# Optimization experiments

Measured on AMD Instinct MI355X. Metric: run time of the kernel, lower is better.

The kernel has to match this reference:

```python
import jax, jax.numpy as jnp
import numpy as np

EMB = 768
HEADS = 12
HEAD_DIM = EMB // HEADS
SCALE = HEAD_DIM ** -0.5


def setup_inputs() -> dict:
    key = jax.random.key(0)
    kq, kk, kv, kw = jax.random.split(key, 4)
    B, H, N, D = 2, HEADS, 2048, HEAD_DIM
    queries = jax.random.normal(kq, (B, H, N, D), dtype=jnp.float32)
    keys = jax.random.normal(kk, (B, H, N, D), dtype=jnp.float32)
    values = jax.random.normal(kv, (B, H, N, D), dtype=jnp.float32)
    proj_w = jax.random.normal(kw, (EMB, EMB), dtype=jnp.float32) * (EMB ** -0.5)
    proj_b = jnp.zeros((EMB,), dtype=jnp.float32)
    return {"queries": queries, "keys": keys, "values": values,
            "proj_w": proj_w, "proj_b": proj_b}


def reference(queries, keys, values, proj_w, proj_b):
    # energy: [b, h, n, n] -- full quadratic score matrix, as in the original
    energy = jnp.einsum('bhij,bhkj->bhik', queries, keys) * SCALE
    att = jax.nn.softmax(energy, axis=-1)  # att_drop_p=0.0 -> identity
    out = jnp.einsum('bhij,bhjk->bhik', att, values)  # [b, h, n, d]
    b, h, n, d = out.shape
    out = jnp.transpose(out, (0, 2, 1, 3)).reshape(b, n, h * d)  # 'b h n d -> b n (h d)'
    # nn.Linear: x @ W^T + b (projection dropout is inference identity)
    return out @ proj_w.T + proj_b
```

## Files before the change

kernel.cpp:

```cpp
#include <hip/hip_runtime.h>
#include <cstdint>

typedef short bf16x8 __attribute__((ext_vector_type(8)));
typedef float f32x4 __attribute__((ext_vector_type(4)));
typedef uint16_t u16x4 __attribute__((ext_vector_type(4)));

#define MFMA_16x16x32(a, b, c) __builtin_amdgcn_mfma_f32_16x16x32_bf16((a), (b), (c), 0, 0, 0)

static constexpr int BATCH = 2;
static constexpr int HEADS = 12;
static constexpr int BH    = BATCH * HEADS;
static constexpr int NCTX  = 2048;
static constexpr int DH    = 64;
static constexpr int EMB   = 768;

static constexpr float QSCALE = 0.125f * 1.44269504088896340736f;

__device__ __forceinline__ uint16_t f2bf(float x) {
    uint32_t u = __float_as_uint(x);
    u += 0x7FFFu + ((u >> 16) & 1u);
    return (uint16_t)(u >> 16);
}
__device__ __forceinline__ uint32_t cvt_pk_bf16(float lo, float hi) {
    uint32_t r;
    asm("v_cvt_pk_bf16_f32 %0, %1, %2" : "=v"(r) : "v"(lo), "v"(hi));
    return r;
}

__global__ __launch_bounds__(256) void k_prep(
        const float* __restrict__ v, uint16_t* __restrict__ vt,
        const float* __restrict__ kf32, uint16_t* __restrict__ kb, int n4k,
        const float* __restrict__ w32, uint16_t* __restrict__ wb, int n4w) {
    const int bid = blockIdx.x;
    const int t   = threadIdx.x;

    if (bid < BH * (NCTX / 64)) {
        __shared__ uint16_t tileT[64][72];
        const int bh = bid >> 5;
        const int n0 = (bid & 31) * 64;

        const int r  = t >> 2;
        const int cc = (t & 3) * 16;
        const float* vp = v + ((size_t)bh * NCTX + n0 + r) * DH + cc;
#pragma unroll
        for (int u = 0; u < 4; ++u) {
            float4 x = reinterpret_cast<const float4*>(vp)[u];
            tileT[cc + 4 * u + 0][r] = f2bf(x.x);
            tileT[cc + 4 * u + 1][r] = f2bf(x.y);
            tileT[cc + 4 * u + 2][r] = f2bf(x.z);
            tileT[cc + 4 * u + 3][r] = f2bf(x.w);
        }
        __syncthreads();

        const int l2 = t & 63;
        const int s0 = t >> 6;
        const int gg = l2 >> 4;
        const int c2 = l2 & 15;
        uint16_t* vb = vt + ((size_t)bh * 32 + (n0 >> 6)) * 8 * 512;
#pragma unroll
        for (int u = 0; u < 2; ++u) {
            const int slot = s0 + 4 * u;
            const int f = slot >> 1, h = slot & 1;
            bf16x8 x = *reinterpret_cast<const bf16x8*>(&tileT[f * 16 + c2][h * 32 + 8 * gg]);
            *reinterpret_cast<bf16x8*>(vb + (size_t)slot * 512 + l2 * 8) = x;
        }
    } else {
        const int i = (bid - BH * (NCTX / 64)) * 256 + t;
        const float* src; uint16_t* dst; int j;
        if (i < n4k) { src = kf32; dst = kb; j = i; }
        else {
            j = i - n4k;
            if (j >= n4w) return;
            src = w32; dst = wb;
        }
        float4 x = reinterpret_cast<const float4*>(src)[j];
        u16x4 hv = {f2bf(x.x), f2bf(x.y), f2bf(x.z), f2bf(x.w)};
        reinterpret_cast<u16x4*>(dst)[j] = hv;
    }
}

__global__ __launch_bounds__(256) void k_attn(
        const float* __restrict__ q, const uint16_t* __restrict__ kb,
        const uint16_t* __restrict__ vf, uint16_t* __restrict__ xb) {
    const int bh = blockIdx.y;
    const int b  = bh / HEADS;
    const int h  = bh % HEADS;
    const int tid = threadIdx.x;
    const int w = tid >> 6;
    const int l = tid & 63;
    const int g = l >> 4;
    const int c = l & 15;

    __shared__ uint16_t K_s[2][64][72];
    __shared__ uint16_t P_s[4][16][72];

    const int q0 = blockIdx.x * 64 + w * 16;

    bf16x8 qa[2];
    {
        const float* qp = q + ((size_t)bh * NCTX + q0 + c) * DH + 8 * g;
#pragma unroll
        for (int kf = 0; kf < 2; ++kf) {
            float4 x0 = *reinterpret_cast<const float4*>(qp + kf * 32);
            float4 x1 = *reinterpret_cast<const float4*>(qp + kf * 32 + 4);
            bf16x8 f;
            f[0] = (short)f2bf(x0.x * QSCALE); f[1] = (short)f2bf(x0.y * QSCALE);
            f[2] = (short)f2bf(x0.z * QSCALE); f[3] = (short)f2bf(x0.w * QSCALE);
            f[4] = (short)f2bf(x1.x * QSCALE); f[5] = (short)f2bf(x1.y * QSCALE);
            f[6] = (short)f2bf(x1.z * QSCALE); f[7] = (short)f2bf(x1.w * QSCALE);
            qa[kf] = f;
        }
    }

    f32x4 zero = {0.f, 0.f, 0.f, 0.f};
    f32x4 o[4] = {zero, zero, zero, zero};
    float m = -1e30f;
    float lsum = 0.f;

    const int srow = tid >> 3;
    const int sch  = tid & 7;

    const uint16_t* kb_b = kb + (size_t)bh * NCTX * DH + srow * DH + sch * 8;
    const uint16_t* vf_b = vf + (size_t)bh * 32 * 8 * 512 + (size_t)l * 8;

    {
        bf16x8 a0 = *reinterpret_cast<const bf16x8*>(kb_b);
        bf16x8 a1 = *reinterpret_cast<const bf16x8*>(kb_b + 32 * DH);
        *reinterpret_cast<bf16x8*>(&K_s[0][srow][sch * 8])      = a0;
        *reinterpret_cast<bf16x8*>(&K_s[0][srow + 32][sch * 8]) = a1;
    }
    __syncthreads();

    for (int t = 0; t < NCTX / 64; ++t) {
        const int cur = t & 1;
        const int nxt = cur ^ 1;

        bf16x8 nk0, nk1;
        const bool pf = (t + 1) < NCTX / 64;
        if (pf) {
            const size_t ko = (size_t)(t + 1) * 64 * DH;
            nk0 = *reinterpret_cast<const bf16x8*>(kb_b + ko);
            nk1 = *reinterpret_cast<const bf16x8*>(kb_b + ko + 32 * DH);
        }

        bf16x8 vr[8];
#pragma unroll
        for (int s = 0; s < 8; ++s)
            vr[s] = *reinterpret_cast<const bf16x8*>(vf_b + ((size_t)t * 8 + s) * 512);

        f32x4 s[4] = {zero, zero, zero, zero};
        __builtin_amdgcn_s_setprio(1);
#pragma unroll
        for (int nf = 0; nf < 4; ++nf) {
#pragma unroll
            for (int kf = 0; kf < 2; ++kf) {
                bf16x8 bhf = *reinterpret_cast<const bf16x8*>(&K_s[cur][nf * 16 + c][kf * 32 + 8 * g]);
                s[nf] = MFMA_16x16x32(bhf, qa[kf], s[nf]);
            }
        }
        __builtin_amdgcn_s_setprio(0);

        float pm0 = fmaxf(fmaxf(s[0][0], s[0][1]), fmaxf(s[0][2], s[0][3]));
        float pm1 = fmaxf(fmaxf(s[1][0], s[1][1]), fmaxf(s[1][2], s[1][3]));
        float pm2 = fmaxf(fmaxf(s[2][0], s[2][1]), fmaxf(s[2][2], s[2][3]));
        float pm3 = fmaxf(fmaxf(s[3][0], s[3][1]), fmaxf(s[3][2], s[3][3]));
        float pmax = fmaxf(fmaxf(pm0, pm1), fmaxf(pm2, pm3));

        if (!__all(pmax <= m + 11.0f)) {
            float smax = fmaxf(pmax, __shfl_xor(pmax, 16));
            smax = fmaxf(smax, __shfl_xor(smax, 32));
            float mnew = fmaxf(m, smax);
            float corr = __builtin_amdgcn_exp2f(m - mnew);
            m = mnew;
            lsum *= corr;
#pragma unroll
            for (int r = 0; r < 4; ++r) {
                float cr = __shfl(corr, 4 * g + r);
#pragma unroll
                for (int f = 0; f < 4; ++f) o[f][r] *= cr;
            }
        }

#pragma unroll
        for (int nf = 0; nf < 4; ++nf) {
            float p0 = __builtin_amdgcn_exp2f(s[nf][0] - m);
            float p1 = __builtin_amdgcn_exp2f(s[nf][1] - m);
            float p2 = __builtin_amdgcn_exp2f(s[nf][2] - m);
            float p3 = __builtin_amdgcn_exp2f(s[nf][3] - m);
            lsum += (p0 + p1) + (p2 + p3);
            uint2 pk;
            pk.x = cvt_pk_bf16(p0, p1);
            pk.y = cvt_pk_bf16(p2, p3);
            *reinterpret_cast<uint2*>(&P_s[w][c][16 * nf + 4 * g]) = pk;
        }

        bf16x8 pa0 = *reinterpret_cast<const bf16x8*>(&P_s[w][c][8 * g]);
        bf16x8 pa1 = *reinterpret_cast<const bf16x8*>(&P_s[w][c][32 + 8 * g]);
        __builtin_amdgcn_s_setprio(1);
#pragma unroll
        for (int f = 0; f < 4; ++f) {
            o[f] = MFMA_16x16x32(pa0, vr[2 * f],     o[f]);
            o[f] = MFMA_16x16x32(pa1, vr[2 * f + 1], o[f]);
        }
        __builtin_amdgcn_s_setprio(0);

        if (pf) {
            *reinterpret_cast<bf16x8*>(&K_s[nxt][srow][sch * 8])      = nk0;
            *reinterpret_cast<bf16x8*>(&K_s[nxt][srow + 32][sch * 8]) = nk1;
        }
        __syncthreads();
    }

    lsum += __shfl_xor(lsum, 16);
    lsum += __shfl_xor(lsum, 32);
    const float linv = 1.0f / lsum;

    const size_t xbase = ((size_t)b * NCTX + q0) * EMB + h * DH;
#pragma unroll
    for (int r = 0; r < 4; ++r) {
        float lr = __shfl(linv, 4 * g + r);
#pragma unroll
        for (int f = 0; f < 4; ++f) {
            float v = o[f][r] * lr;
            size_t addr = xbase + (size_t)(4 * g + r) * EMB + f * 16 + c;
            xb[addr] = f2bf(v);
        }
    }
}

__global__ __launch_bounds__(256) void k_proj(
        const uint16_t* __restrict__ xb, const uint16_t* __restrict__ wb,
        const float* __restrict__ bias, float* __restrict__ out) {
    const int tid = threadIdx.x;
    const int w = tid >> 6;
    const int l = tid & 63;
    const int g = l >> 4;
    const int c = l & 15;
    const int m0 = blockIdx.x * 64 + w * 16;
    const int n0 = blockIdx.y * 64;

    __shared__ uint16_t W_s[64][72];

    f32x4 zero = {0.f, 0.f, 0.f, 0.f};
    f32x4 acc[4] = {zero, zero, zero, zero};

    const int srow = tid >> 2;
    const int sch  = tid & 3;
    constexpr int ROUNDS = EMB / 64;

    const uint16_t* whp = wb + (size_t)(n0 + srow) * EMB + sch * 8;
    const uint16_t* xhp = xb + (size_t)(m0 + c) * EMB + 8 * g;

    bf16x8 w0 = *reinterpret_cast<const bf16x8*>(whp);
    bf16x8 w1 = *reinterpret_cast<const bf16x8*>(whp + 32);
    bf16x8 a0 = *reinterpret_cast<const bf16x8*>(xhp);
    bf16x8 a1 = *reinterpret_cast<const bf16x8*>(xhp + 32);

    for (int rd = 0; rd < ROUNDS; ++rd) {
        __syncthreads();
        *reinterpret_cast<bf16x8*>(&W_s[srow][sch * 8])      = w0;
        *reinterpret_cast<bf16x8*>(&W_s[srow][32 + sch * 8]) = w1;
        __syncthreads();

        const int rn = (rd + 1 < ROUNDS) ? (rd + 1) : (ROUNDS - 1);
        bf16x8 w0n = *reinterpret_cast<const bf16x8*>(whp + (size_t)rn * 64);
        bf16x8 w1n = *reinterpret_cast<const bf16x8*>(whp + (size_t)rn * 64 + 32);
        bf16x8 a0n = *reinterpret_cast<const bf16x8*>(xhp + (size_t)rn * 64);
        bf16x8 a1n = *reinterpret_cast<const bf16x8*>(xhp + (size_t)rn * 64 + 32);

        __builtin_amdgcn_s_setprio(1);
#pragma unroll
        for (int nf = 0; nf < 4; ++nf) {
            bf16x8 b0 = *reinterpret_cast<const bf16x8*>(&W_s[nf * 16 + c][8 * g]);
            bf16x8 b1 = *reinterpret_cast<const bf16x8*>(&W_s[nf * 16 + c][32 + 8 * g]);
            acc[nf] = MFMA_16x16x32(a0, b0, acc[nf]);
            acc[nf] = MFMA_16x16x32(a1, b1, acc[nf]);
        }
        __builtin_amdgcn_s_setprio(0);

        w0 = w0n; w1 = w1n; a0 = a0n; a1 = a1n;
    }

#pragma unroll
    for (int nf = 0; nf < 4; ++nf) {
#pragma unroll
        for (int r = 0; r < 4; ++r) {
            int row = m0 + g * 4 + r;
            int col = n0 + nf * 16 + c;
            out[(size_t)row * EMB + col] = acc[nf][r] + bias[col];
        }
    }
}

extern "C" void kernel_launch(void* const* d_in, const int* in_sizes, int n_in,
                              void* d_out, int out_size, void* d_ws, size_t ws_size,
                              hipStream_t stream) {
    const float* q    = (const float*)d_in[0];
    const float* k    = (const float*)d_in[1];
    const float* v    = (const float*)d_in[2];
    const float* pw   = (const float*)d_in[3];
    const float* pb   = (const float*)d_in[4];
    float* out = (float*)d_out;

    const size_t nqkv = (size_t)BH * NCTX * DH;
    const size_t nx   = (size_t)BATCH * NCTX * EMB;
    const size_t nw   = (size_t)EMB * EMB;

    uint8_t* ws = (uint8_t*)d_ws;
    uint16_t* kb = (uint16_t*)ws;              ws += nqkv * 2;
    uint16_t* vf = (uint16_t*)ws;              ws += nqkv * 2;
    uint16_t* xb = (uint16_t*)ws;              ws += nx * 2;
    uint16_t* wb = (uint16_t*)ws;              ws += nw * 2;

    const int n4k = (int)(nqkv / 4);
    const int n4w = (int)(nw / 4);
    const int nprep = BH * (NCTX / 64) + (n4k + n4w + 255) / 256;
    k_prep<<<nprep, 256, 0, stream>>>(v, vf, k, kb, n4k, pw, wb, n4w);

    k_attn<<<dim3(NCTX / 64, BH), 256, 0, stream>>>(q, kb, vf, xb);

    k_proj<<<dim3((BATCH * NCTX) / 64, EMB / 64), 256, 0, stream>>>(xb, wb, pb, out);
}
```

Before: 74.83 us.

## Pre-swizzle K into MFMA fragment layout and load it directly into registers

The prep kernel now writes K in bf16 in the same per-lane MFMA fragment order already used for V. The attention kernel then drops the shared-memory K double buffer and the per-tile __syncthreads, and instead prefetches the next tile's K fragments from global memory straight into registers. This removes LDS traffic and block-wide barriers from the inner loop. In exchange each wave now loads K itself, so K traffic to L2 rises by the number of waves per block, and more registers are in use.

```diff
diff --git a/kernel.cpp b/kernel.cpp
--- a/kernel.cpp
+++ b/kernel.cpp
@@ -13,6 +13,7 @@
 static constexpr int NCTX  = 2048;
 static constexpr int DH    = 64;
 static constexpr int EMB   = 768;
+static constexpr int NT    = NCTX / 64;
 
 static constexpr float QSCALE = 0.125f * 1.44269504088896340736f;
 
@@ -29,12 +30,13 @@
 
 __global__ __launch_bounds__(256) void k_prep(
         const float* __restrict__ v, uint16_t* __restrict__ vt,
-        const float* __restrict__ kf32, uint16_t* __restrict__ kb, int n4k,
+        const float* __restrict__ kf32, uint16_t* __restrict__ kfr,
         const float* __restrict__ w32, uint16_t* __restrict__ wb, int n4w) {
     const int bid = blockIdx.x;
     const int t   = threadIdx.x;
-
-    if (bid < BH * (NCTX / 64)) {
+    constexpr int NVB = BH * NT;
+
+    if (bid < NVB) {
         __shared__ uint16_t tileT[64][72];
         const int bh = bid >> 5;
         const int n0 = (bid & 31) * 64;
@@ -64,23 +66,41 @@
             bf16x8 x = *reinterpret_cast<const bf16x8*>(&tileT[f * 16 + c2][h * 32 + 8 * gg]);
             *reinterpret_cast<bf16x8*>(vb + (size_t)slot * 512 + l2 * 8) = x;
         }
+    } else if (bid < 2 * NVB) {
+        const int kb2 = bid - NVB;
+        const int bh = kb2 >> 5;
+        const int n0 = (kb2 & 31) * 64;
+        const int l2 = t & 63;
+        const int s0 = t >> 6;
+        const int gg = l2 >> 4;
+        const int c2 = l2 & 15;
+        uint16_t* kb = kfr + ((size_t)bh * 32 + (n0 >> 6)) * 8 * 512;
+#pragma unroll
+        for (int u = 0; u < 2; ++u) {
+            const int slot = s0 + 4 * u;
+            const int nf = slot >> 1, kf = slot & 1;
+            const float* kp = kf32 + ((size_t)bh * NCTX + n0 + 16 * nf + c2) * DH
+                                   + 32 * kf + 8 * gg;
+            float4 x0 = *reinterpret_cast<const float4*>(kp);
+            float4 x1 = *reinterpret_cast<const float4*>(kp + 4);
+            bf16x8 f;
+            f[0] = (short)f2bf(x0.x); f[1] = (short)f2bf(x0.y);
+            f[2] = (short)f2bf(x0.z); f[3] = (short)f2bf(x0.w);
+            f[4] = (short)f2bf(x1.x); f[5] = (short)f2bf(x1.y);
+            f[6] = (short)f2bf(x1.z); f[7] = (short)f2bf(x1.w);
+            *reinterpret_cast<bf16x8*>(kb + (size_t)slot * 512 + l2 * 8) = f;
+        }
     } else {
-        const int i = (bid - BH * (NCTX / 64)) * 256 + t;
-        const float* src; uint16_t* dst; int j;
-        if (i < n4k) { src = kf32; dst = kb; j = i; }
-        else {
-            j = i - n4k;
-            if (j >= n4w) return;
-            src = w32; dst = wb;
-        }
-        float4 x = reinterpret_cast<const float4*>(src)[j];
+        const int i = (bid - 2 * NVB) * 256 + t;
+        if (i >= n4w) return;
+        float4 x = reinterpret_cast<const float4*>(w32)[i];
         u16x4 hv = {f2bf(x.x), f2bf(x.y), f2bf(x.z), f2bf(x.w)};
-        reinterpret_cast<u16x4*>(dst)[j] = hv;
+        reinterpret_cast<u16x4*>(wb)[i] = hv;
     }
 }
 
 __global__ __launch_bounds__(256) void k_attn(
-        const float* __restrict__ q, const uint16_t* __restrict__ kb,
+        const float* __restrict__ q, const uint16_t* __restrict__ kfr,
         const uint16_t* __restrict__ vf, uint16_t* __restrict__ xb) {
     const int bh = blockIdx.y;
     const int b  = bh / HEADS;
@@ -91,7 +111,6 @@
     const int g = l >> 4;
     const int c = l & 15;
 
-    __shared__ uint16_t K_s[2][64][72];
     __shared__ uint16_t P_s[4][16][72];
 
     const int q0 = blockIdx.x * 64 + w * 16;
@@ -117,48 +136,36 @@
     float m = -1e30f;
     float lsum = 0.f;
 
-    const int srow = tid >> 3;
-    const int sch  = tid & 7;
-
-    const uint16_t* kb_b = kb + (size_t)bh * NCTX * DH + srow * DH + sch * 8;
-    const uint16_t* vf_b = vf + (size_t)bh * 32 * 8 * 512 + (size_t)l * 8;
-
-    {
-        bf16x8 a0 = *reinterpret_cast<const bf16x8*>(kb_b);
-        bf16x8 a1 = *reinterpret_cast<const bf16x8*>(kb_b + 32 * DH);
-        *reinterpret_cast<bf16x8*>(&K_s[0][srow][sch * 8])      = a0;
-        *reinterpret_cast<bf16x8*>(&K_s[0][srow + 32][sch * 8]) = a1;
-    }
-    __syncthreads();
-
-    for (int t = 0; t < NCTX / 64; ++t) {
-        const int cur = t & 1;
-        const int nxt = cur ^ 1;
-
-        bf16x8 nk0, nk1;
-        const bool pf = (t + 1) < NCTX / 64;
-        if (pf) {
-            const size_t ko = (size_t)(t + 1) * 64 * DH;
-            nk0 = *reinterpret_cast<const bf16x8*>(kb_b + ko);
-            nk1 = *reinterpret_cast<const bf16x8*>(kb_b + ko + 32 * DH);
-        }
-
+    const uint16_t* kf_b = kfr + (size_t)bh * 32 * 8 * 512 + (size_t)l * 8;
+    const uint16_t* vf_b = vf  + (size_t)bh * 32 * 8 * 512 + (size_t)l * 8;
+
+    bf16x8 kr[8];
+#pragma unroll
+    for (int s2 = 0; s2 < 8; ++s2)
+        kr[s2] = *reinterpret_cast<const bf16x8*>(kf_b + (size_t)s2 * 512);
+
+    for (int t = 0; t < NT; ++t) {
         bf16x8 vr[8];
 #pragma unroll
-        for (int s = 0; s < 8; ++s)
-            vr[s] = *reinterpret_cast<const bf16x8*>(vf_b + ((size_t)t * 8 + s) * 512);
+        for (int s2 = 0; s2 < 8; ++s2)
+            vr[s2] = *reinterpret_cast<const bf16x8*>(vf_b + ((size_t)t * 8 + s2) * 512);
 
         f32x4 s[4] = {zero, zero, zero, zero};
         __builtin_amdgcn_s_setprio(1);
 #pragma unroll
         for (int nf = 0; nf < 4; ++nf) {
 #pragma unroll
-            for (int kf = 0; kf < 2; ++kf) {
-                bf16x8 bhf = *reinterpret_cast<const bf16x8*>(&K_s[cur][nf * 16 + c][kf * 32 + 8 * g]);
-                s[nf] = MFMA_16x16x32(bhf, qa[kf], s[nf]);
-            }
+            for (int kf = 0; kf < 2; ++kf)
+                s[nf] = MFMA_16x16x32(kr[2 * nf + kf], qa[kf], s[nf]);
         }
         __builtin_amdgcn_s_setprio(0);
+
+        {
+            const int tn = (t + 1 < NT) ? (t + 1) : (NT - 1);
+#pragma unroll
+            for (int s2 = 0; s2 < 8; ++s2)
+                kr[s2] = *reinterpret_cast<const bf16x8*>(kf_b + ((size_t)tn * 8 + s2) * 512);
+        }
 
         float pm0 = fmaxf(fmaxf(s[0][0], s[0][1]), fmaxf(s[0][2], s[0][3]));
         float pm1 = fmaxf(fmaxf(s[1][0], s[1][1]), fmaxf(s[1][2], s[1][3]));
@@ -203,12 +210,6 @@
             o[f] = MFMA_16x16x32(pa1, vr[2 * f + 1], o[f]);
         }
         __builtin_amdgcn_s_setprio(0);
-
-        if (pf) {
-            *reinterpret_cast<bf16x8*>(&K_s[nxt][srow][sch * 8])      = nk0;
-            *reinterpret_cast<bf16x8*>(&K_s[nxt][srow + 32][sch * 8]) = nk1;
-        }
-        __syncthreads();
     }
 
     lsum += __shfl_xor(lsum, 16);
@@ -307,17 +308,16 @@
     const size_t nw   = (size_t)EMB * EMB;
 
     uint8_t* ws = (uint8_t*)d_ws;
-    uint16_t* kb = (uint16_t*)ws;              ws += nqkv * 2;
-    uint16_t* vf = (uint16_t*)ws;              ws += nqkv * 2;
-    uint16_t* xb = (uint16_t*)ws;              ws += nx * 2;
-    uint16_t* wb = (uint16_t*)ws;              ws += nw * 2;
-
-    const int n4k = (int)(nqkv / 4);
+    uint16_t* kfr = (uint16_t*)ws;             ws += nqkv * 2;
+    uint16_t* vfr = (uint16_t*)ws;             ws += nqkv * 2;
+    uint16_t* xb  = (uint16_t*)ws;             ws += nx * 2;
+    uint16_t* wb  = (uint16_t*)ws;             ws += nw * 2;
+
     const int n4w = (int)(nw / 4);
-    const int nprep = BH * (NCTX / 64) + (n4k + n4w + 255) / 256;
-    k_prep<<<nprep, 256, 0, stream>>>(v, vf, k, kb, n4k, pw, wb, n4w);
-
-    k_attn<<<dim3(NCTX / 64, BH), 256, 0, stream>>>(q, kb, vf, xb);
+    const int nprep = 2 * BH * NT + (n4w + 255) / 256;
+    k_prep<<<nprep, 256, 0, stream>>>(v, vfr, k, kfr, pw, wb, n4w);
+
+    k_attn<<<dim3(NCTX / 64, BH), 256, 0, stream>>>(q, kfr, vfr, xb);
 
     k_proj<<<dim3((BATCH * NCTX) / 64, EMB / 64), 256, 0, stream>>>(xb, wb, pb, out);
 }
```

New measurement: 79.29 us. +6.0%, slower.
